# Performance work log

Hardware: AMD Instinct MI355X
Metric: run time of the kernel (lower is better)

Reference implementation:

```python
import jax, jax.numpy as jnp
import numpy as np

NUM_HEADS = 6
LOCAL_KS = 3


def setup_inputs() -> dict:
    key = jax.random.key(0)
    k1, k2, k3, k4 = jax.random.split(key, 4)
    B, N, C = 8, 1024, 384
    x = jax.random.normal(k1, (B, N, C), dtype=jnp.float32)
    qkv_w = jax.random.normal(k2, (3 * C, C), dtype=jnp.float32) * (C ** -0.5)
    proj_w = jax.random.normal(k3, (C, C), dtype=jnp.float32) * (C ** -0.5)
    proj_b = jax.random.normal(k4, (C,), dtype=jnp.float32) * 0.01
    return {"x": x, "qkv_w": qkv_w, "proj_w": proj_w, "proj_b": proj_b}


def reference(x, qkv_w, proj_w, proj_b):
    B, N, C = x.shape
    H = NUM_HEADS
    hd = C // H
    scale = hd ** -0.5
    half = LOCAL_KS // 2

    # qkv projection: [B,N,3C] -> q,k,v each [B,H,N,hd]
    qkv = (x @ qkv_w.T).reshape(B, N, 3, H, hd).transpose(2, 0, 3, 1, 4)
    q, k, v = qkv[0], qkv[1], qkv[2]

    # dense scores with banded local mask (clamped window == |i-j| <= half)
    attn = jnp.einsum('bhqd,bhkd->bhqk', q, k) * scale
    idx = jnp.arange(N)
    mask = jnp.abs(idx[:, None] - idx[None, :]) > half  # True -> masked out
    attn = jnp.where(mask, -jnp.inf, attn)
    p = jax.nn.softmax(attn, axis=-1)

    # AV then merge heads: [B,N,C]
    out = jnp.einsum('bhqk,bhkd->bqhd', p, v).reshape(B, N, C)
    return out @ proj_w.T + proj_b
```

## Files before the change

### kernel.cpp

```cpp
#include <hip/hip_runtime.h>
#include <hip/hip_bf16.h>
#include <math.h>

#define C_DIM 384
#define NHEADS 6
#define HD 64
#define BATCH 8
#define NSEQ 1024
#define M_ROWS (BATCH * NSEQ)

typedef __attribute__((ext_vector_type(4))) float f32x4;
typedef __attribute__((ext_vector_type(8))) short s16x8;

__device__ __forceinline__ float bf2f(short u) {
  return __uint_as_float(((unsigned)(unsigned short)u) << 16);
}
__device__ __forceinline__ short f2bf(float f) {
  __hip_bfloat16 h = __float2bfloat16(f);
  return *reinterpret_cast<short*>(&h);
}

__device__ __forceinline__ void gload_lds16(const void* g, void* l) {
  __builtin_amdgcn_global_load_lds(
      (const __attribute__((address_space(1))) unsigned int*)g,
      (__attribute__((address_space(3))) unsigned int*)l, 16, 0, 0);
}

__global__ __launch_bounds__(256) void cast_all(
    const float* __restrict__ x, const float* __restrict__ qw,
    const float* __restrict__ pw,
    ushort4* __restrict__ xo, ushort4* __restrict__ qo, ushort4* __restrict__ po) {
  const int NX = M_ROWS * C_DIM / 4;
  const int NQ = 3 * C_DIM * C_DIM / 4;
  const int NP = C_DIM * C_DIM / 4;
  const int total = NX + NQ + NP;
  int idx = blockIdx.x * blockDim.x + threadIdx.x;
  int stride = gridDim.x * blockDim.x;
  for (int i = idx; i < total; i += stride) {
    const float4* s;
    ushort4* d;
    int off;
    if (i < NX) { s = (const float4*)x; d = xo; off = i; }
    else if (i < NX + NQ) { s = (const float4*)qw; d = qo; off = i - NX; }
    else { s = (const float4*)pw; d = po; off = i - NX - NQ; }
    float4 v = s[off];
    ushort4 o;
    o.x = (unsigned short)f2bf(v.x);
    o.y = (unsigned short)f2bf(v.y);
    o.z = (unsigned short)f2bf(v.z);
    o.w = (unsigned short)f2bf(v.w);
    d[off] = o;
  }
}

template<bool OUT_BF16>
__global__ __launch_bounds__(256) void gemm_bf16_nt(
    const __hip_bfloat16* __restrict__ A,
    const __hip_bfloat16* __restrict__ W,
    const float* __restrict__ bias,
    void* __restrict__ outp,
    int M, int N, int K) {
  __shared__ __align__(16) __hip_bfloat16 As[128 * 32];
  __shared__ __align__(16) __hip_bfloat16 Bs[128 * 32];

  const int tid = threadIdx.x;
  const int lane = tid & 63;
  const int wave = tid >> 6;
  const int wr = (wave >> 1) * 64;
  const int wc = (wave & 1) * 64;
  const int rowBase = blockIdx.y * 128;
  const int colBase = blockIdx.x * 128;

  const int l16 = lane & 15;
  const int lk8 = (lane >> 4) * 8;
  const int lr4 = (lane >> 4) * 4;

  f32x4 acc[4][4] = {};

  const int nkt = K >> 5;
  for (int kt = 0; kt < nkt; ++kt) {
    const int k0 = kt * 32;
#pragma unroll
    for (int i = 0; i < 2; ++i) {
      int c = tid + i * 256;
      int r = c >> 2;
      int cc = (c & 3) * 8;
      gload_lds16(A + (size_t)(rowBase + r) * K + k0 + cc, As + c * 8);
      gload_lds16(W + (size_t)(colBase + r) * K + k0 + cc, Bs + c * 8);
    }
    __syncthreads();

    s16x8 af[4], bf[4];
#pragma unroll
    for (int m = 0; m < 4; ++m)
      af[m] = *(const s16x8*)(As + (wr + m * 16 + l16) * 32 + lk8);
#pragma unroll
    for (int n = 0; n < 4; ++n)
      bf[n] = *(const s16x8*)(Bs + (wc + n * 16 + l16) * 32 + lk8);
#pragma unroll
    for (int m = 0; m < 4; ++m)
#pragma unroll
      for (int n = 0; n < 4; ++n)
        acc[m][n] = __builtin_amdgcn_mfma_f32_16x16x32_bf16(
            af[m], bf[n], acc[m][n], 0, 0, 0);
    __syncthreads();
  }

#pragma unroll
  for (int m = 0; m < 4; ++m) {
    int rb = rowBase + wr + m * 16 + lr4;
#pragma unroll
    for (int n = 0; n < 4; ++n) {
      int cb = colBase + wc + n * 16 + l16;
#pragma unroll
      for (int j = 0; j < 4; ++j) {
        float v = acc[m][n][j];
        if (OUT_BF16) {
          ((__hip_bfloat16*)outp)[(size_t)(rb + j) * N + cb] = __float2bfloat16(v);
        } else {
          ((float*)outp)[(size_t)(rb + j) * N + cb] = v + bias[cb];
        }
      }
    }
  }
}

__global__ __launch_bounds__(256) void local_attn_v3(
    const __hip_bfloat16* __restrict__ qkv, __hip_bfloat16* __restrict__ attn_out) {
  __shared__ __align__(16) ushort lds[24832];
  const int QOFF = 0;
  const int KOFF = 8192;
  const int VOFF = 8192 + 8320;

  const int tid = threadIdx.x;
  const int mb = blockIdx.x & 63;
  const int h  = blockIdx.x >> 6;
  const int rb = mb * 128;
  const int b  = rb >> 10;
  const int n0 = rb & 1023;
  const int RS = 3 * C_DIM;

#pragma unroll
  for (int i = 0; i < 4; ++i) {
    int s = i * 256 + tid;
    int r = s >> 3;
    int jg = (s & 7) ^ (r & 7);
    gload_lds16(qkv + (size_t)(rb + r) * RS + h * HD + jg * 8,
                lds + QOFF + s * 8);
  }
#pragma unroll
  for (int i = 0; i < 5; ++i) {
    int s = i * 256 + tid;
    if (s < 1040) {
      int r = s >> 3;
      int jg = (s & 7) ^ (r & 7);
      int nl = n0 + r - 1;
      nl = nl < 0 ? 0 : (nl > 1023 ? 1023 : nl);
      size_t row = (size_t)(b << 10) + nl;
      gload_lds16(qkv + row * RS + C_DIM + h * HD + jg * 8, lds + KOFF + s * 8);
      gload_lds16(qkv + row * RS + 2 * C_DIM + h * HD + jg * 8, lds + VOFF + s * 8);
    }
  }
  __syncthreads();

  const int r = tid >> 1;
  const int half = tid & 1;
  const int jbase = half * 4;
  const int n = n0 + r;

  float qf[32];
#pragma unroll
  for (int c = 0; c < 4; ++c) {
    int slot = r * 8 + ((jbase + c) ^ (r & 7));
    s16x8 v = *(const s16x8*)(lds + QOFF + slot * 8);
#pragma unroll
    for (int e = 0; e < 8; ++e) qf[c * 8 + e] = bf2f(v[e]);
  }

  float s3[3];
#pragma unroll
  for (int jj = 0; jj < 3; ++jj) {
    int krow = r + jj;
    float acc = 0.f;
#pragma unroll
    for (int c = 0; c < 4; ++c) {
      int slot = krow * 8 + ((jbase + c) ^ (krow & 7));
      s16x8 v = *(const s16x8*)(lds + KOFF + slot * 8);
#pragma unroll
      for (int e = 0; e < 8; ++e) acc += qf[c * 8 + e] * bf2f(v[e]);
    }
    acc += __shfl_xor(acc, 1);
    s3[jj] = ((unsigned)(n + jj - 1) < (unsigned)NSEQ) ? acc * 0.125f : -1e30f;
  }

  float mx = fmaxf(s3[0], fmaxf(s3[1], s3[2]));
  float p0 = __expf(s3[0] - mx);
  float p1 = __expf(s3[1] - mx);
  float p2 = __expf(s3[2] - mx);
  float inv = 1.f / (p0 + p1 + p2);
  float p[3] = {p0 * inv, p1 * inv, p2 * inv};

  float of[32] = {};
#pragma unroll
  for (int jj = 0; jj < 3; ++jj) {
    int krow = r + jj;
    float pw = p[jj];
#pragma unroll
    for (int c = 0; c < 4; ++c) {
      int slot = krow * 8 + ((jbase + c) ^ (krow & 7));
      s16x8 v = *(const s16x8*)(lds + VOFF + slot * 8);
#pragma unroll
      for (int e = 0; e < 8; ++e) of[c * 8 + e] += pw * bf2f(v[e]);
    }
  }

#pragma unroll
  for (int c = 0; c < 4; ++c) {
    s16x8 o;
#pragma unroll
    for (int e = 0; e < 8; ++e) o[e] = f2bf(of[c * 8 + e]);
    *(s16x8*)(attn_out + (size_t)(rb + r) * C_DIM + h * HD + jbase * 8 + c * 8) = o;
  }
}

extern "C" void kernel_launch(void* const* d_in, const int* in_sizes, int n_in,
                              void* d_out, int out_size, void* d_ws, size_t ws_size,
                              hipStream_t stream) {
  const float* x      = (const float*)d_in[0];
  const float* qkv_w  = (const float*)d_in[1];
  const float* proj_w = (const float*)d_in[2];
  const float* proj_b = (const float*)d_in[3];
  float* out = (float*)d_out;

  __hip_bfloat16* x_bf     = (__hip_bfloat16*)d_ws;
  __hip_bfloat16* qkvw_bf  = x_bf + (size_t)M_ROWS * C_DIM;
  __hip_bfloat16* projw_bf = qkvw_bf + (size_t)3 * C_DIM * C_DIM;
  __hip_bfloat16* qkv_bf   = projw_bf + (size_t)C_DIM * C_DIM;
  __hip_bfloat16* attn_bf  = qkv_bf + (size_t)M_ROWS * 3 * C_DIM;

  cast_all<<<1024, 256, 0, stream>>>(
      x, qkv_w, proj_w, (ushort4*)x_bf, (ushort4*)qkvw_bf, (ushort4*)projw_bf);

  gemm_bf16_nt<true><<<dim3((3 * C_DIM) / 128, M_ROWS / 128), 256, 0, stream>>>(
      x_bf, qkvw_bf, nullptr, qkv_bf, M_ROWS, 3 * C_DIM, C_DIM);

  local_attn_v3<<<64 * NHEADS, 256, 0, stream>>>(qkv_bf, attn_bf);

  gemm_bf16_nt<false><<<dim3(C_DIM / 128, M_ROWS / 128), 256, 0, stream>>>(
      attn_bf, projw_bf, proj_b, out, M_ROWS, C_DIM, C_DIM);
}
```

Before: 50.21 us.

## Double-buffer GEMM LDS tiles, remap workgroups across XCDs, narrow proj tile

The GEMM now double-buffers its LDS tiles: it prefetches the next K-slice with global_load_lds and waits on vmcnt with explicit barriers, so loads overlap MFMA work. Workgroup IDs are remapped so that consecutive tiles land on the same XCD, which should improve L2 reuse. The output projection uses a 64-wide N tile to launch more workgroups for the small 384-column GEMM. The cost is twice the LDS and reliance on hand-tuned vmcnt counts, which are correct only if the compiler emits exactly the expected number of loads.

After: 43.98 us. -12.4%, faster.

```diff
diff --git a/kernel.cpp b/kernel.cpp
--- a/kernel.cpp
+++ b/kernel.cpp
@@ -24,6 +24,12 @@
   __builtin_amdgcn_global_load_lds(
       (const __attribute__((address_space(1))) unsigned int*)g,
       (__attribute__((address_space(3))) unsigned int*)l, 16, 0, 0);
+}
+
+template<int N> __device__ __forceinline__ void wait_vm() {
+  if constexpr (N == 0) asm volatile("s_waitcnt vmcnt(0)" ::: "memory");
+  else if constexpr (N == 3) asm volatile("s_waitcnt vmcnt(3)" ::: "memory");
+  else if constexpr (N == 4) asm volatile("s_waitcnt vmcnt(4)" ::: "memory");
 }
 
 __global__ __launch_bounds__(256) void cast_all(
@@ -53,64 +59,95 @@
   }
 }
 
-template<bool OUT_BF16>
-__global__ __launch_bounds__(256) void gemm_bf16_nt(
+template<int BN, bool OUT_BF16>
+__global__ __launch_bounds__(256) void gemm_db(
     const __hip_bfloat16* __restrict__ A,
     const __hip_bfloat16* __restrict__ W,
     const float* __restrict__ bias,
     void* __restrict__ outp,
     int M, int N, int K) {
-  __shared__ __align__(16) __hip_bfloat16 As[128 * 32];
-  __shared__ __align__(16) __hip_bfloat16 Bs[128 * 32];
+  constexpr int NF = BN / 32;
+  constexpr int BPT = (BN * 32 / 8) / 256;
+  constexpr int LPS = 2 + BPT;
+  __shared__ __align__(16) __hip_bfloat16 As[2][128 * 32];
+  __shared__ __align__(16) __hip_bfloat16 Bs[2][BN * 32];
 
   const int tid = threadIdx.x;
+  const int nwg = gridDim.x * gridDim.y;
+  const int bid0 = blockIdx.y * gridDim.x + blockIdx.x;
+  const int cpx = nwg >> 3;
+  const int wg = (bid0 & 7) * cpx + (bid0 >> 3);
+  const int bx = wg % gridDim.x;
+  const int by = wg / gridDim.x;
+
   const int lane = tid & 63;
   const int wave = tid >> 6;
   const int wr = (wave >> 1) * 64;
-  const int wc = (wave & 1) * 64;
-  const int rowBase = blockIdx.y * 128;
-  const int colBase = blockIdx.x * 128;
+  const int wc = (wave & 1) * (BN / 2);
+  const int rowBase = by * 128;
+  const int colBase = bx * BN;
 
   const int l16 = lane & 15;
   const int lk8 = (lane >> 4) * 8;
   const int lr4 = (lane >> 4) * 4;
 
-  f32x4 acc[4][4] = {};
+  f32x4 acc[4][NF] = {};
 
   const int nkt = K >> 5;
-  for (int kt = 0; kt < nkt; ++kt) {
+
+  auto stage = [&](int buf, int kt) {
     const int k0 = kt * 32;
 #pragma unroll
     for (int i = 0; i < 2; ++i) {
       int c = tid + i * 256;
-      int r = c >> 2;
-      int cc = (c & 3) * 8;
-      gload_lds16(A + (size_t)(rowBase + r) * K + k0 + cc, As + c * 8);
-      gload_lds16(W + (size_t)(colBase + r) * K + k0 + cc, Bs + c * 8);
-    }
-    __syncthreads();
-
-    s16x8 af[4], bf[4];
+      int r = c >> 2, cc = (c & 3) * 8;
+      gload_lds16(A + (size_t)(rowBase + r) * K + k0 + cc, &As[buf][c * 8]);
+    }
+#pragma unroll
+    for (int i = 0; i < BPT; ++i) {
+      int c = tid + i * 256;
+      int r = c >> 2, cc = (c & 3) * 8;
+      gload_lds16(W + (size_t)(colBase + r) * K + k0 + cc, &Bs[buf][c * 8]);
+    }
+  };
+
+  stage(0, 0);
+  for (int kt = 0; kt < nkt; ++kt) {
+    const int cur = kt & 1;
+    if (kt + 1 < nkt) {
+      stage(cur ^ 1, kt + 1);
+      wait_vm<LPS>();
+    } else {
+      wait_vm<0>();
+    }
+    __builtin_amdgcn_sched_barrier(0);
+    __builtin_amdgcn_s_barrier();
+    __builtin_amdgcn_sched_barrier(0);
+
+    s16x8 af[4], bfr[NF];
 #pragma unroll
     for (int m = 0; m < 4; ++m)
-      af[m] = *(const s16x8*)(As + (wr + m * 16 + l16) * 32 + lk8);
-#pragma unroll
-    for (int n = 0; n < 4; ++n)
-      bf[n] = *(const s16x8*)(Bs + (wc + n * 16 + l16) * 32 + lk8);
+      af[m] = *(const s16x8*)(&As[cur][(wr + m * 16 + l16) * 32 + lk8]);
+#pragma unroll
+    for (int n = 0; n < NF; ++n)
+      bfr[n] = *(const s16x8*)(&Bs[cur][(wc + n * 16 + l16) * 32 + lk8]);
 #pragma unroll
     for (int m = 0; m < 4; ++m)
 #pragma unroll
-      for (int n = 0; n < 4; ++n)
+      for (int n = 0; n < NF; ++n)
         acc[m][n] = __builtin_amdgcn_mfma_f32_16x16x32_bf16(
-            af[m], bf[n], acc[m][n], 0, 0, 0);
-    __syncthreads();
+            af[m], bfr[n], acc[m][n], 0, 0, 0);
+
+    __builtin_amdgcn_sched_barrier(0);
+    __builtin_amdgcn_s_barrier();
+    __builtin_amdgcn_sched_barrier(0);
   }
 
 #pragma unroll
   for (int m = 0; m < 4; ++m) {
     int rb = rowBase + wr + m * 16 + lr4;
 #pragma unroll
-    for (int n = 0; n < 4; ++n) {
+    for (int n = 0; n < NF; ++n) {
       int cb = colBase + wc + n * 16 + l16;
 #pragma unroll
       for (int j = 0; j < 4; ++j) {
@@ -241,11 +278,11 @@
   cast_all<<<1024, 256, 0, stream>>>(
       x, qkv_w, proj_w, (ushort4*)x_bf, (ushort4*)qkvw_bf, (ushort4*)projw_bf);
 
-  gemm_bf16_nt<true><<<dim3((3 * C_DIM) / 128, M_ROWS / 128), 256, 0, stream>>>(
+  gemm_db<128, true><<<dim3((3 * C_DIM) / 128, M_ROWS / 128), 256, 0, stream>>>(
       x_bf, qkvw_bf, nullptr, qkv_bf, M_ROWS, 3 * C_DIM, C_DIM);
 
   local_attn_v3<<<64 * NHEADS, 256, 0, stream>>>(qkv_bf, attn_bf);
 
-  gemm_bf16_nt<false><<<dim3(C_DIM / 128, M_ROWS / 128), 256, 0, stream>>>(
+  gemm_db<64, false><<<dim3(C_DIM / 64, M_ROWS / 128), 256, 0, stream>>>(
       attn_bf, projw_bf, proj_b, out, M_ROWS, C_DIM, C_DIM);
 }
```

## Fuse fp32-to-bf16 casts into GEMMs with whole-K weight tiles resident in LDS

Applied to the files above, without the earlier changes.

Removes the separate cast kernel. Each GEMM workgroup converts and stages its whole 64-column weight slice (full K=384, padded stride) in LDS once. The A operand is read straight from global, with fp32 x converted in registers. The K loop then runs without per-iteration syncs, and block IDs are remapped in groups of 8 for locality. In exchange, each workgroup recasts the weights redundantly, the tile shrinks to 128x64, and A loads go global-to-register with no LDS staging.

Result: slower. 93.05 us (+85.3%).

```diff
diff --git a/kernel.cpp b/kernel.cpp
--- a/kernel.cpp
+++ b/kernel.cpp
@@ -8,6 +8,7 @@
 #define BATCH 8
 #define NSEQ 1024
 #define M_ROWS (BATCH * NSEQ)
+#define BLDP 392
 
 typedef __attribute__((ext_vector_type(4))) float f32x4;
 typedef __attribute__((ext_vector_type(8))) short s16x8;
@@ -18,6 +19,12 @@
 __device__ __forceinline__ short f2bf(float f) {
   __hip_bfloat16 h = __float2bfloat16(f);
   return *reinterpret_cast<short*>(&h);
+}
+__device__ __forceinline__ s16x8 cvt8(float4 a, float4 b) {
+  s16x8 r;
+  r[0] = f2bf(a.x); r[1] = f2bf(a.y); r[2] = f2bf(a.z); r[3] = f2bf(a.w);
+  r[4] = f2bf(b.x); r[5] = f2bf(b.y); r[6] = f2bf(b.z); r[7] = f2bf(b.w);
+  return r;
 }
 
 __device__ __forceinline__ void gload_lds16(const void* g, void* l) {
@@ -26,99 +33,84 @@
       (__attribute__((address_space(3))) unsigned int*)l, 16, 0, 0);
 }
 
-__global__ __launch_bounds__(256) void cast_all(
-    const float* __restrict__ x, const float* __restrict__ qw,
-    const float* __restrict__ pw,
-    ushort4* __restrict__ xo, ushort4* __restrict__ qo, ushort4* __restrict__ po) {
-  const int NX = M_ROWS * C_DIM / 4;
-  const int NQ = 3 * C_DIM * C_DIM / 4;
-  const int NP = C_DIM * C_DIM / 4;
-  const int total = NX + NQ + NP;
-  int idx = blockIdx.x * blockDim.x + threadIdx.x;
-  int stride = gridDim.x * blockDim.x;
-  for (int i = idx; i < total; i += stride) {
-    const float4* s;
-    ushort4* d;
-    int off;
-    if (i < NX) { s = (const float4*)x; d = xo; off = i; }
-    else if (i < NX + NQ) { s = (const float4*)qw; d = qo; off = i - NX; }
-    else { s = (const float4*)pw; d = po; off = i - NX - NQ; }
-    float4 v = s[off];
-    ushort4 o;
-    o.x = (unsigned short)f2bf(v.x);
-    o.y = (unsigned short)f2bf(v.y);
-    o.z = (unsigned short)f2bf(v.z);
-    o.w = (unsigned short)f2bf(v.w);
-    d[off] = o;
-  }
-}
-
-template<bool OUT_BF16>
-__global__ __launch_bounds__(256) void gemm_bf16_nt(
-    const __hip_bfloat16* __restrict__ A,
-    const __hip_bfloat16* __restrict__ W,
-    const float* __restrict__ bias,
-    void* __restrict__ outp,
+template<bool A_BF16, bool OUT_BF16>
+__global__ __launch_bounds__(256) void gemm_bstat(
+    const void* __restrict__ Ap, const float* __restrict__ W,
+    const float* __restrict__ bias, void* __restrict__ outp,
     int M, int N, int K) {
-  __shared__ __align__(16) __hip_bfloat16 As[128 * 32];
-  __shared__ __align__(16) __hip_bfloat16 Bs[128 * 32];
+  __shared__ __align__(16) __hip_bfloat16 Bs[64 * BLDP];
 
   const int tid = threadIdx.x;
+  const int nwg = gridDim.x * gridDim.y;
+  const int bid0 = blockIdx.y * gridDim.x + blockIdx.x;
+  const int cpx = nwg >> 3;
+  const int wg = (bid0 & 7) * cpx + (bid0 >> 3);
+  const int bx = wg % gridDim.x;
+  const int by = wg / gridDim.x;
+
   const int lane = tid & 63;
   const int wave = tid >> 6;
   const int wr = (wave >> 1) * 64;
-  const int wc = (wave & 1) * 64;
-  const int rowBase = blockIdx.y * 128;
-  const int colBase = blockIdx.x * 128;
-
+  const int wc = (wave & 1) * 32;
+  const int rowBase = by * 128;
+  const int colBase = bx * 64;
   const int l16 = lane & 15;
   const int lk8 = (lane >> 4) * 8;
   const int lr4 = (lane >> 4) * 4;
 
-  f32x4 acc[4][4] = {};
-
+#pragma unroll
+  for (int i = 0; i < 6; ++i) {
+    int c = tid + i * 256;
+    int row = c / 24;
+    int col = (c % 24) * 16;
+    const float4* src = (const float4*)(W + (size_t)(colBase + row) * K + col);
+    float4 u0 = src[0], u1 = src[1], u2 = src[2], u3 = src[3];
+    *(s16x8*)&Bs[row * BLDP + col]     = cvt8(u0, u1);
+    *(s16x8*)&Bs[row * BLDP + col + 8] = cvt8(u2, u3);
+  }
+  __syncthreads();
+
+  f32x4 acc[4][2] = {};
   const int nkt = K >> 5;
+
+#pragma unroll 2
   for (int kt = 0; kt < nkt; ++kt) {
-    const int k0 = kt * 32;
-#pragma unroll
-    for (int i = 0; i < 2; ++i) {
-      int c = tid + i * 256;
-      int r = c >> 2;
-      int cc = (c & 3) * 8;
-      gload_lds16(A + (size_t)(rowBase + r) * K + k0 + cc, As + c * 8);
-      gload_lds16(W + (size_t)(colBase + r) * K + k0 + cc, Bs + c * 8);
-    }
-    __syncthreads();
-
-    s16x8 af[4], bf[4];
+    s16x8 af[4], bfr[2];
+#pragma unroll
+    for (int m = 0; m < 4; ++m) {
+      size_t rowOff = (size_t)(rowBase + wr + m * 16 + l16) * K + kt * 32 + lk8;
+      if constexpr (A_BF16) {
+        af[m] = *(const s16x8*)((const __hip_bfloat16*)Ap + rowOff);
+      } else {
+        const float4* ap = (const float4*)((const float*)Ap + rowOff);
+        af[m] = cvt8(ap[0], ap[1]);
+      }
+    }
+#pragma unroll
+    for (int n = 0; n < 2; ++n)
+      bfr[n] = *(const s16x8*)(&Bs[(wc + n * 16 + l16) * BLDP + kt * 32 + lk8]);
 #pragma unroll
     for (int m = 0; m < 4; ++m)
-      af[m] = *(const s16x8*)(As + (wr + m * 16 + l16) * 32 + lk8);
-#pragma unroll
-    for (int n = 0; n < 4; ++n)
-      bf[n] = *(const s16x8*)(Bs + (wc + n * 16 + l16) * 32 + lk8);
-#pragma unroll
-    for (int m = 0; m < 4; ++m)
-#pragma unroll
-      for (int n = 0; n < 4; ++n)
+#pragma unroll
+      for (int n = 0; n < 2; ++n)
         acc[m][n] = __builtin_amdgcn_mfma_f32_16x16x32_bf16(
-            af[m], bf[n], acc[m][n], 0, 0, 0);
-    __syncthreads();
+            af[m], bfr[n], acc[m][n], 0, 0, 0);
   }
 
 #pragma unroll
   for (int m = 0; m < 4; ++m) {
     int rb = rowBase + wr + m * 16 + lr4;
 #pragma unroll
-    for (int n = 0; n < 4; ++n) {
+    for (int n = 0; n < 2; ++n) {
       int cb = colBase + wc + n * 16 + l16;
+      float bv = OUT_BF16 ? 0.f : bias[cb];
 #pragma unroll
       for (int j = 0; j < 4; ++j) {
-        float v = acc[m][n][j];
-        if (OUT_BF16) {
-          ((__hip_bfloat16*)outp)[(size_t)(rb + j) * N + cb] = __float2bfloat16(v);
+        if constexpr (OUT_BF16) {
+          ((__hip_bfloat16*)outp)[(size_t)(rb + j) * N + cb] =
+              __float2bfloat16(acc[m][n][j]);
         } else {
-          ((float*)outp)[(size_t)(rb + j) * N + cb] = v + bias[cb];
+          ((float*)outp)[(size_t)(rb + j) * N + cb] = acc[m][n][j] + bv;
         }
       }
     }
@@ -232,20 +224,14 @@
   const float* proj_b = (const float*)d_in[3];
   float* out = (float*)d_out;
 
-  __hip_bfloat16* x_bf     = (__hip_bfloat16*)d_ws;
-  __hip_bfloat16* qkvw_bf  = x_bf + (size_t)M_ROWS * C_DIM;
-  __hip_bfloat16* projw_bf = qkvw_bf + (size_t)3 * C_DIM * C_DIM;
-  __hip_bfloat16* qkv_bf   = projw_bf + (size_t)C_DIM * C_DIM;
-  __hip_bfloat16* attn_bf  = qkv_bf + (size_t)M_ROWS * 3 * C_DIM;
-
-  cast_all<<<1024, 256, 0, stream>>>(
-      x, qkv_w, proj_w, (ushort4*)x_bf, (ushort4*)qkvw_bf, (ushort4*)projw_bf);
-
-  gemm_bf16_nt<true><<<dim3((3 * C_DIM) / 128, M_ROWS / 128), 256, 0, stream>>>(
-      x_bf, qkvw_bf, nullptr, qkv_bf, M_ROWS, 3 * C_DIM, C_DIM);
+  __hip_bfloat16* qkv_bf  = (__hip_bfloat16*)d_ws;
+  __hip_bfloat16* attn_bf = qkv_bf + (size_t)M_ROWS * 3 * C_DIM;
+
+  gemm_bstat<false, true><<<dim3(18, 64), 256, 0, stream>>>(
+      x, qkv_w, nullptr, qkv_bf, M_ROWS, 3 * C_DIM, C_DIM);
 
   local_attn_v3<<<64 * NHEADS, 256, 0, stream>>>(qkv_bf, attn_bf);
 
-  gemm_bf16_nt<false><<<dim3(C_DIM / 128, M_ROWS / 128), 256, 0, stream>>>(
-      attn_bf, projw_bf, proj_b, out, M_ROWS, C_DIM, C_DIM);
-}
+  gemm_bstat<true, false><<<dim3(6, 64), 256, 0, stream>>>(
+      attn_bf, proj_w, proj_b, out, M_ROWS, C_DIM, C_DIM);
+}
```
